# Kernel tuning notes

Hardware: AMD Instinct MI355X
Metric: run time of the kernel (lower is better)

## Reference

```python
import jax, jax.numpy as jnp
import numpy as np

FEATURE_DIM = 128
BATCH = 2
SEQ = 512  # single domain region (0, SEQ) per batch element


def setup_inputs() -> dict:
    key = jax.random.key(0)
    ks = jax.random.split(key, 8)
    D = FEATURE_DIM
    s = lambda fan_in: 1.0 / np.sqrt(fan_in)
    return {
        "domain_features": jax.random.normal(ks[0], (BATCH, SEQ, D), jnp.float32),
        "evolutionary_features": jax.random.normal(ks[1], (BATCH, SEQ, D), jnp.float32),
        # pattern_detector params (jax convention: W is [in, out])
        "W1": jax.random.uniform(ks[2], (2 * D, D), jnp.float32, -s(2 * D), s(2 * D)),
        "b1": jax.random.uniform(ks[3], (D,), jnp.float32, -s(2 * D), s(2 * D)),
        "W2": jax.random.uniform(ks[4], (D, D // 2), jnp.float32, -s(D), s(D)),
        "b2": jax.random.uniform(ks[5], (D // 2,), jnp.float32, -s(D), s(D)),
        "W3": jax.random.uniform(ks[6], (D // 2, 1), jnp.float32, -s(D // 2), s(D // 2)),
        "b3": jax.random.uniform(ks[7], (1,), jnp.float32, -s(D // 2), s(D // 2)),
    }


def reference(domain_features, evolutionary_features, W1, b1, W2, b2, W3, b3):
    D = domain_features.shape[-1]
    # per-position combined feature: g_i = domain_feat[i] * evo_feat[i]
    g = domain_features * evolutionary_features  # [B, N, D]
    # Linear(2D -> D) on cat(g_i, g_j) splits into two halves of W1
    a = jnp.einsum("bnd,de->bne", g, W1[:D])  # contribution of position i
    c = jnp.einsum("bnd,de->bne", g, W1[D:])  # contribution of position j
    h = jax.nn.relu(a[:, :, None, :] + c[:, None, :, :] + b1)       # [B, N, N, D]
    h = jax.nn.relu(jnp.einsum("bijd,de->bije", h, W2) + b2)        # [B, N, N, D//2]
    s = jax.nn.sigmoid(jnp.einsum("bije,e->bij", h, W3[:, 0]) + b3[0])  # [B, N, N]
    # original loop fills only i < j and mirrors; diagonal stays zero
    upper = jnp.triu(s, k=1)
    coevo = upper + jnp.swapaxes(upper, -1, -2)  # symmetric [B, N, N]
    return coevo
```

## Files before the change

### kernel.cpp

```cpp
#include <hip/hip_runtime.h>
#include <hip/hip_bf16.h>

#define D 128
#define Nn 512
#define Bb 2

typedef __bf16 bf16x8_t __attribute__((ext_vector_type(8)));
typedef unsigned short u16x8_t __attribute__((ext_vector_type(8)));
typedef float f32x4_t __attribute__((ext_vector_type(4)));
typedef float f32x8_t __attribute__((ext_vector_type(8)));

__global__ __launch_bounds__(256)
void precompute_ac(const float* __restrict__ dom, const float* __restrict__ evo,
                   const float* __restrict__ W1, const float* __restrict__ b1,
                   const float* __restrict__ W2,
                   float* __restrict__ A, __bf16* __restrict__ Cb,
                   __bf16* __restrict__ W2T) {
    const int t = threadIdx.x;
    const int base = blockIdx.x * 4;
    if (blockIdx.x < 8) {
#pragma unroll
        for (int z = 0; z < 4; ++z) {
            int idx = z * 256 + t;
            int e = blockIdx.x * 8 + (idx >> 7);
            int k = idx & 127;
            W2T[e * 128 + k] = (__bf16)W2[k * 64 + e];
        }
    }
    __shared__ float g4[4][D];
#pragma unroll
    for (int it = 0; it < 2; ++it) {
        int idx = it * 256 + t;
        int r = idx >> 7, c = idx & 127;
        size_t off = (size_t)(base + r) * D + c;
        g4[r][c] = dom[off] * evo[off];
    }
    __syncthreads();
    const int half = t >> 7;
    const int e = t & 127;
    const float* Wp = W1 + half * D * D;
    float a0 = 0.f, a1 = 0.f, a2 = 0.f, a3 = 0.f;
#pragma unroll 8
    for (int dp = 0; dp < D; ++dp) {
        float w = Wp[dp * D + e];
        a0 = fmaf(g4[0][dp], w, a0);
        a1 = fmaf(g4[1][dp], w, a1);
        a2 = fmaf(g4[2][dp], w, a2);
        a3 = fmaf(g4[3][dp], w, a3);
    }
    if (half == 0) {
        float bb = b1[e];
        A[(size_t)(base + 0) * D + e] = a0 + bb;
        A[(size_t)(base + 1) * D + e] = a1 + bb;
        A[(size_t)(base + 2) * D + e] = a2 + bb;
        A[(size_t)(base + 3) * D + e] = a3 + bb;
    } else {
        Cb[(size_t)(base + 0) * D + e] = (__bf16)a0;
        Cb[(size_t)(base + 1) * D + e] = (__bf16)a1;
        Cb[(size_t)(base + 2) * D + e] = (__bf16)a2;
        Cb[(size_t)(base + 3) * D + e] = (__bf16)a3;
    }
}

__global__ __launch_bounds__(256, 4)
void coevo_main(const float* __restrict__ A, const __bf16* __restrict__ Cm,
                const __bf16* __restrict__ W2T, const float* __restrict__ b2,
                const float* __restrict__ W3, const float* __restrict__ b3,
                float* __restrict__ out) {
    const int tid  = threadIdx.x;
    const int wave = tid >> 6;
    const int lane = tid & 63;
    const int m = lane & 15;
    const int q = lane >> 4;

    int u = blockIdx.x;
    const int b = (u >= 576) ? 1 : 0;
    u -= b * 576;
    int chunk = 0;
#pragma unroll
    for (int cc = 1; cc < 8; ++cc) if (u >= 8 * cc * (cc + 1)) chunk = cc;
    const int g = u - 8 * chunk * (chunk + 1);
    const int i = g * 4 + wave;
    const int i0 = g * 4;

    __shared__ __bf16 cs[64 * 128];
    __shared__ __bf16 w2s[64 * 128];
    __shared__ float  tile[4][64];

    const f32x4_t* Cg = (const f32x4_t*)(Cm + ((size_t)b * Nn + (size_t)chunk * 64) * D);
    f32x4_t* csv = (f32x4_t*)cs;
#pragma unroll
    for (int it = 0; it < 4; ++it) {
        int f = it * 256 + tid;
        int r = f >> 4, gi = f & 15;
        csv[r * 16 + (gi ^ (r & 15))] = Cg[f];
    }
    f32x4_t* w2v = (f32x4_t*)w2s;
    const f32x4_t* W2Tg = (const f32x4_t*)W2T;
#pragma unroll
    for (int it = 0; it < 4; ++it) {
        int f = it * 256 + tid;
        int r = f >> 4, gi = f & 15;
        w2v[r * 16 + (gi ^ (r & 15))] = W2Tg[f];
    }

    f32x8_t abv[4];
    {
        const float* Ap = A + ((size_t)(b * Nn + i)) * D + q * 8;
#pragma unroll
        for (int kk = 0; kk < 4; ++kk) {
            f32x4_t v0 = *(const f32x4_t*)(Ap + kk * 32);
            f32x4_t v1 = *(const f32x4_t*)(Ap + kk * 32 + 4);
            f32x8_t v;
            v[0] = v0[0]; v[1] = v0[1]; v[2] = v0[2]; v[3] = v0[3];
            v[4] = v1[0]; v[5] = v1[1]; v[6] = v1[2]; v[7] = v1[3];
            abv[kk] = v;
        }
    }

    float b2v[4], w3v[4];
#pragma unroll
    for (int et = 0; et < 4; ++et) {
        b2v[et] = b2[et * 16 + m];
        w3v[et] = W3[et * 16 + m];
    }
    const float b3s = b3[0];

    __syncthreads();

    const u16x8_t* csr  = (const u16x8_t*)cs;
    const bf16x8_t* w2r = (const bf16x8_t*)w2s;

#pragma unroll
    for (int jt = 0; jt < 4; ++jt) {
        if (chunk * 64 + jt * 16 + 15 < i) continue;
        const int r0  = jt * 16 + m;
        const int key = r0 & 15;

        bf16x8_t af[4];
#pragma unroll
        for (int kk = 0; kk < 4; ++kk) {
            u16x8_t cr = csr[r0 * 16 + ((kk * 4 + q) ^ key)];
            f32x8_t c8;
#pragma unroll
            for (int z = 0; z < 8; ++z)
                c8[z] = __builtin_bit_cast(float, (unsigned)cr[z] << 16);
            f32x8_t t8 = __builtin_elementwise_max(abv[kk] + c8, (f32x8_t)0.f);
            af[kk] = __builtin_convertvector(t8, bf16x8_t);
        }

        float part[4] = {0.f, 0.f, 0.f, 0.f};
#pragma unroll
        for (int et = 0; et < 4; ++et) {
            bf16x8_t wf[4];
#pragma unroll
            for (int kk = 0; kk < 4; ++kk)
                wf[kk] = w2r[(et * 16 + m) * 16 + ((kk * 4 + q) ^ m)];
            f32x4_t a = {0.f, 0.f, 0.f, 0.f};
#pragma unroll
            for (int kk = 0; kk < 4; ++kk)
                a = __builtin_amdgcn_mfma_f32_16x16x32_bf16(af[kk], wf[kk], a, 0, 0, 0);
#pragma unroll
            for (int r = 0; r < 4; ++r)
                part[r] = fmaf(fmaxf(a[r] + b2v[et], 0.f), w3v[et], part[r]);
        }

#pragma unroll
        for (int off = 8; off >= 1; off >>= 1) {
#pragma unroll
            for (int r = 0; r < 4; ++r)
                part[r] += __shfl_xor(part[r], off, 64);
        }
        if (m == 0) {
#pragma unroll
            for (int r = 0; r < 4; ++r) {
                int jc = jt * 16 + q * 4 + r;
                tile[wave][jc] = 1.f / (1.f + expf(-(part[r] + b3s)));
            }
        }
    }

    __syncthreads();

    if ((tid & 63) < 16) {
        const int c4 = tid & 15;
        const int j0 = chunk * 64 + c4 * 4;
        float v0 = tile[wave][c4 * 4 + 0];
        float v1 = tile[wave][c4 * 4 + 1];
        float v2 = tile[wave][c4 * 4 + 2];
        float v3 = tile[wave][c4 * 4 + 3];
        float* op = out + ((size_t)b * Nn + i) * Nn + j0;
        if (j0 > i) {
            f32x4_t v; v[0] = v0; v[1] = v1; v[2] = v2; v[3] = v3;
            *(f32x4_t*)op = v;
        } else if (j0 + 3 >= i) {
            if (j0 + 0 > i) op[0] = v0; else if (j0 + 0 == i) op[0] = 0.f;
            if (j0 + 1 > i) op[1] = v1; else if (j0 + 1 == i) op[1] = 0.f;
            if (j0 + 2 > i) op[2] = v2; else if (j0 + 2 == i) op[2] = 0.f;
            if (j0 + 3 > i) op[3] = v3; else if (j0 + 3 == i) op[3] = 0.f;
        }
    }
    if (tid < 64) {
        const int j = chunk * 64 + tid;
        float v0 = tile[0][tid], v1 = tile[1][tid], v2 = tile[2][tid], v3 = tile[3][tid];
        float* op = out + ((size_t)b * Nn + j) * Nn + i0;
        if (j > i0 + 3) {
            f32x4_t v; v[0] = v0; v[1] = v1; v[2] = v2; v[3] = v3;
            *(f32x4_t*)op = v;
        } else {
            if (j > i0 + 0) op[0] = v0;
            if (j > i0 + 1) op[1] = v1;
            if (j > i0 + 2) op[2] = v2;
            if (j > i0 + 3) op[3] = v3;
        }
    }
}

extern "C" void kernel_launch(void* const* d_in, const int* in_sizes, int n_in,
                              void* d_out, int out_size, void* d_ws, size_t ws_size,
                              hipStream_t stream) {
    const float* dom = (const float*)d_in[0];
    const float* evo = (const float*)d_in[1];
    const float* W1  = (const float*)d_in[2];
    const float* b1  = (const float*)d_in[3];
    const float* W2  = (const float*)d_in[4];
    const float* b2  = (const float*)d_in[5];
    const float* W3  = (const float*)d_in[6];
    const float* b3  = (const float*)d_in[7];
    float* out = (float*)d_out;

    float*  A   = (float*)d_ws;
    __bf16* Cb  = (__bf16*)(A + (size_t)Bb * Nn * D);
    __bf16* W2T = Cb + (size_t)Bb * Nn * D;

    precompute_ac<<<Bb * Nn / 4, 256, 0, stream>>>(dom, evo, W1, b1, W2, A, Cb, W2T);
    coevo_main<<<Bb * 576, 256, 0, stream>>>(A, Cb, W2T, b2, W3, b3, out);
}
```

Baseline: 26.23 us.

## Keep C in fp32 LDS, stream W2 from global, batch jt tiles, DPP reduce

C is now stored in fp32 instead of bf16, which removes the bf16-to-fp32 unpack and changes the LDS swizzle to 32-vector rows. W2T is no longer staged in shared memory: each lane reads its fragments straight from global memory into double-buffered registers. The loop is restructured so that all four j-tiles' A fragments are built first, then each W2 fragment is reused across the tiles. The shuffle reduction is replaced with DPP row reductions, and launch bounds drop occupancy from 4 to 3. The costs are more global traffic for C, higher register pressure from af[4][4] and part[4][4], and a numerics change because C is no longer rounded to bf16.

```diff
diff --git a/kernel.cpp b/kernel.cpp
--- a/kernel.cpp
+++ b/kernel.cpp
@@ -6,7 +6,6 @@
 #define Bb 2
 
 typedef __bf16 bf16x8_t __attribute__((ext_vector_type(8)));
-typedef unsigned short u16x8_t __attribute__((ext_vector_type(8)));
 typedef float f32x4_t __attribute__((ext_vector_type(4)));
 typedef float f32x8_t __attribute__((ext_vector_type(8)));
 
@@ -14,7 +13,7 @@
 void precompute_ac(const float* __restrict__ dom, const float* __restrict__ evo,
                    const float* __restrict__ W1, const float* __restrict__ b1,
                    const float* __restrict__ W2,
-                   float* __restrict__ A, __bf16* __restrict__ Cb,
+                   float* __restrict__ A, float* __restrict__ C,
                    __bf16* __restrict__ W2T) {
     const int t = threadIdx.x;
     const int base = blockIdx.x * 4;
@@ -40,7 +39,7 @@
     const int e = t & 127;
     const float* Wp = W1 + half * D * D;
     float a0 = 0.f, a1 = 0.f, a2 = 0.f, a3 = 0.f;
-#pragma unroll 8
+#pragma unroll 16
     for (int dp = 0; dp < D; ++dp) {
         float w = Wp[dp * D + e];
         a0 = fmaf(g4[0][dp], w, a0);
@@ -55,15 +54,27 @@
         A[(size_t)(base + 2) * D + e] = a2 + bb;
         A[(size_t)(base + 3) * D + e] = a3 + bb;
     } else {
-        Cb[(size_t)(base + 0) * D + e] = (__bf16)a0;
-        Cb[(size_t)(base + 1) * D + e] = (__bf16)a1;
-        Cb[(size_t)(base + 2) * D + e] = (__bf16)a2;
-        Cb[(size_t)(base + 3) * D + e] = (__bf16)a3;
-    }
-}
-
-__global__ __launch_bounds__(256, 4)
-void coevo_main(const float* __restrict__ A, const __bf16* __restrict__ Cm,
+        C[(size_t)(base + 0) * D + e] = a0;
+        C[(size_t)(base + 1) * D + e] = a1;
+        C[(size_t)(base + 2) * D + e] = a2;
+        C[(size_t)(base + 3) * D + e] = a3;
+    }
+}
+
+__device__ __forceinline__ float row16_reduce(float x) {
+    int v = __builtin_bit_cast(int, x);
+    x += __builtin_bit_cast(float, __builtin_amdgcn_update_dpp(0, v, 0x118, 0xf, 0xf, false));
+    v = __builtin_bit_cast(int, x);
+    x += __builtin_bit_cast(float, __builtin_amdgcn_update_dpp(0, v, 0x114, 0xf, 0xf, false));
+    v = __builtin_bit_cast(int, x);
+    x += __builtin_bit_cast(float, __builtin_amdgcn_update_dpp(0, v, 0x112, 0xf, 0xf, false));
+    v = __builtin_bit_cast(int, x);
+    x += __builtin_bit_cast(float, __builtin_amdgcn_update_dpp(0, v, 0x111, 0xf, 0xf, false));
+    return x;
+}
+
+__global__ __launch_bounds__(256, 3)
+void coevo_main(const float* __restrict__ A, const float* __restrict__ Cm,
                 const __bf16* __restrict__ W2T, const float* __restrict__ b2,
                 const float* __restrict__ W3, const float* __restrict__ b3,
                 float* __restrict__ out) {
@@ -83,25 +94,16 @@
     const int i = g * 4 + wave;
     const int i0 = g * 4;
 
-    __shared__ __bf16 cs[64 * 128];
-    __shared__ __bf16 w2s[64 * 128];
-    __shared__ float  tile[4][64];
+    __shared__ float cs[64 * 128];
+    __shared__ float tile[4][64];
 
     const f32x4_t* Cg = (const f32x4_t*)(Cm + ((size_t)b * Nn + (size_t)chunk * 64) * D);
     f32x4_t* csv = (f32x4_t*)cs;
 #pragma unroll
-    for (int it = 0; it < 4; ++it) {
+    for (int it = 0; it < 8; ++it) {
         int f = it * 256 + tid;
-        int r = f >> 4, gi = f & 15;
-        csv[r * 16 + (gi ^ (r & 15))] = Cg[f];
-    }
-    f32x4_t* w2v = (f32x4_t*)w2s;
-    const f32x4_t* W2Tg = (const f32x4_t*)W2T;
-#pragma unroll
-    for (int it = 0; it < 4; ++it) {
-        int f = it * 256 + tid;
-        int r = f >> 4, gi = f & 15;
-        w2v[r * 16 + (gi ^ (r & 15))] = W2Tg[f];
+        int r = f >> 5, gi = f & 31;
+        csv[r * 32 + (gi ^ (r & 7))] = Cg[f];
     }
 
     f32x8_t abv[4];
@@ -128,54 +130,66 @@
 
     __syncthreads();
 
-    const u16x8_t* csr  = (const u16x8_t*)cs;
-    const bf16x8_t* w2r = (const bf16x8_t*)w2s;
-
+    bool act[4];
+    bf16x8_t af[4][4];
 #pragma unroll
     for (int jt = 0; jt < 4; ++jt) {
-        if (chunk * 64 + jt * 16 + 15 < i) continue;
+        act[jt] = (chunk * 64 + jt * 16 + 15 >= i);
+        if (!act[jt]) continue;
         const int r0  = jt * 16 + m;
-        const int key = r0 & 15;
-
-        bf16x8_t af[4];
+        const int key = r0 & 7;
+        const f32x4_t* base = (const f32x4_t*)cs + r0 * 32;
 #pragma unroll
         for (int kk = 0; kk < 4; ++kk) {
-            u16x8_t cr = csr[r0 * 16 + ((kk * 4 + q) ^ key)];
+            const int g0 = kk * 8 + q * 2;
+            f32x4_t c0 = base[g0 ^ key];
+            f32x4_t c1 = base[(g0 + 1) ^ key];
             f32x8_t c8;
-#pragma unroll
-            for (int z = 0; z < 8; ++z)
-                c8[z] = __builtin_bit_cast(float, (unsigned)cr[z] << 16);
+            c8[0] = c0[0]; c8[1] = c0[1]; c8[2] = c0[2]; c8[3] = c0[3];
+            c8[4] = c1[0]; c8[5] = c1[1]; c8[6] = c1[2]; c8[7] = c1[3];
             f32x8_t t8 = __builtin_elementwise_max(abv[kk] + c8, (f32x8_t)0.f);
-            af[kk] = __builtin_convertvector(t8, bf16x8_t);
-        }
-
-        float part[4] = {0.f, 0.f, 0.f, 0.f};
-#pragma unroll
-        for (int et = 0; et < 4; ++et) {
-            bf16x8_t wf[4];
+            af[jt][kk] = __builtin_convertvector(t8, bf16x8_t);
+        }
+    }
+
+    const bf16x8_t* W2g = (const bf16x8_t*)W2T;
+    bf16x8_t wf[2][4];
+#pragma unroll
+    for (int kk = 0; kk < 4; ++kk)
+        wf[0][kk] = W2g[(0 * 16 + m) * 16 + kk * 4 + q];
+
+    float part[4][4] = {{0.f}};
+#pragma unroll
+    for (int et = 0; et < 4; ++et) {
+        if (et < 3) {
 #pragma unroll
             for (int kk = 0; kk < 4; ++kk)
-                wf[kk] = w2r[(et * 16 + m) * 16 + ((kk * 4 + q) ^ m)];
+                wf[(et + 1) & 1][kk] = W2g[((et + 1) * 16 + m) * 16 + kk * 4 + q];
+        }
+#pragma unroll
+        for (int jt = 0; jt < 4; ++jt) {
+            if (!act[jt]) continue;
             f32x4_t a = {0.f, 0.f, 0.f, 0.f};
 #pragma unroll
             for (int kk = 0; kk < 4; ++kk)
-                a = __builtin_amdgcn_mfma_f32_16x16x32_bf16(af[kk], wf[kk], a, 0, 0, 0);
+                a = __builtin_amdgcn_mfma_f32_16x16x32_bf16(af[jt][kk], wf[et & 1][kk], a, 0, 0, 0);
 #pragma unroll
             for (int r = 0; r < 4; ++r)
-                part[r] = fmaf(fmaxf(a[r] + b2v[et], 0.f), w3v[et], part[r]);
-        }
-
-#pragma unroll
-        for (int off = 8; off >= 1; off >>= 1) {
-#pragma unroll
-            for (int r = 0; r < 4; ++r)
-                part[r] += __shfl_xor(part[r], off, 64);
-        }
-        if (m == 0) {
+                part[jt][r] = fmaf(fmaxf(a[r] + b2v[et], 0.f), w3v[et], part[jt][r]);
+        }
+    }
+
+#pragma unroll
+    for (int jt = 0; jt < 4; ++jt) {
+        if (!act[jt]) continue;
+        float red[4];
+#pragma unroll
+        for (int r = 0; r < 4; ++r) red[r] = row16_reduce(part[jt][r]);
+        if (m == 15) {
 #pragma unroll
             for (int r = 0; r < 4; ++r) {
                 int jc = jt * 16 + q * 4 + r;
-                tile[wave][jc] = 1.f / (1.f + expf(-(part[r] + b3s)));
+                tile[wave][jc] = 1.f / (1.f + expf(-(red[r] + b3s)));
             }
         }
     }
@@ -230,9 +244,9 @@
     float* out = (float*)d_out;
 
     float*  A   = (float*)d_ws;
-    __bf16* Cb  = (__bf16*)(A + (size_t)Bb * Nn * D);
-    __bf16* W2T = Cb + (size_t)Bb * Nn * D;
-
-    precompute_ac<<<Bb * Nn / 4, 256, 0, stream>>>(dom, evo, W1, b1, W2, A, Cb, W2T);
-    coevo_main<<<Bb * 576, 256, 0, stream>>>(A, Cb, W2T, b2, W3, b3, out);
-}
+    float*  C   = A + (size_t)Bb * Nn * D;
+    __bf16* W2T = (__bf16*)(C + (size_t)Bb * Nn * D);
+
+    precompute_ac<<<Bb * Nn / 4, 256, 0, stream>>>(dom, evo, W1, b1, W2, A, C, W2T);
+    coevo_main<<<Bb * 576, 256, 0, stream>>>(A, C, W2T, b2, W3, b3, out);
+}
```

Result: slower. 28.06 us (+7.0%).
